# Kernel tuning notes

Hardware: AMD Instinct MI355X
Metric: run time of the kernel (lower is better)

## Reference

```python
import jax, jax.numpy as jnp
import numpy as np

# ---- dims ----
D_MODEL = 256
HEADDIM = 16          # per-head d_model for each inner Mamba2
NH = D_MODEL // HEADDIM   # 16 DiffMamba heads
D_STATE = 64
D_CONV = 4
EXPAND = 2
D_INNER = EXPAND * HEADDIM        # 32
NH_IN = D_INNER // HEADDIM        # 2 internal mamba2 heads
CONV_DIM = D_INNER + 2 * D_STATE  # 160
D_IN_PROJ = 2 * D_INNER + 2 * D_STATE + NH_IN  # 194
B, T = 2, 2048


def silu(v):
    return v * jax.nn.sigmoid(v)


def mamba2_single(u, Win, convw, convb, dt_bias, A_log, Dp, nw, Wout):
    """Reference Mamba2 forward for one module. u: [B, T, HEADDIM]."""
    Bb, Tt, _ = u.shape
    zxbcdt = u @ Win.T                       # [B, T, D_IN_PROJ]
    z = zxbcdt[..., :D_INNER]
    xBC = zxbcdt[..., D_INNER:D_INNER + CONV_DIM]
    dt = jax.nn.softplus(zxbcdt[..., -NH_IN:] + dt_bias)  # [B, T, NH_IN]
    # causal depthwise conv1d over time (kernel D_CONV)
    xp = jnp.pad(xBC, ((0, 0), (D_CONV - 1, 0), (0, 0)))
    conv = convb + sum(xp[:, k:k + Tt, :] * convw[:, k] for k in range(D_CONV))
    xBC = silu(conv)
    x = xBC[..., :D_INNER].reshape(Bb, Tt, NH_IN, HEADDIM)
    Bm = xBC[..., D_INNER:D_INNER + D_STATE]   # [B, T, N]
    Cm = xBC[..., D_INNER + D_STATE:]          # [B, T, N]
    A = -jnp.exp(A_log)                        # [NH_IN]
    dA = jnp.exp(dt * A)                       # [B, T, NH_IN]
    dBx = jnp.einsum('bth,btn,bthp->bthpn', dt, Bm, x)

    def step(h, inp):
        dA_t, dBx_t, C_t = inp                 # [B,H], [B,H,P,N], [B,N]
        h = dA_t[:, :, None, None] * h + dBx_t
        y = jnp.einsum('bhpn,bn->bhp', h, C_t)
        return h, y

    h0 = jnp.zeros((Bb, NH_IN, HEADDIM, D_STATE), u.dtype)
    xs = (jnp.moveaxis(dA, 1, 0), jnp.moveaxis(dBx, 1, 0), jnp.moveaxis(Cm, 1, 0))
    _, ys = jax.lax.scan(step, h0, xs)         # ys: [T, B, H, P]
    y = jnp.moveaxis(ys, 0, 1) + Dp[None, None, :, None] * x
    y = y.reshape(Bb, Tt, D_INNER)
    # RMSNormGated(norm_before_gate=False): gate then rmsnorm
    y = y * silu(z)
    y = y * jax.lax.rsqrt(jnp.mean(y * y, axis=-1, keepdims=True) + 1e-5) * nw
    return y @ Wout.T                          # [B, T, HEADDIM]


mamba2_v = jax.vmap(mamba2_single)  # over stacked head/module axis


def setup_inputs() -> dict:
    key = jax.random.key(0)

    def team_params(kbase, tag):
        k = jax.random.split(kbase, 6)
        Win = jax.random.uniform(k[0], (NH, D_IN_PROJ, HEADDIM), minval=-0.25, maxval=0.25)
        convw = jax.random.uniform(k[1], (NH, CONV_DIM, D_CONV), minval=-0.5, maxval=0.5)
        convb = jax.random.uniform(k[2], (NH, CONV_DIM), minval=-0.5, maxval=0.5)
        dt = jnp.exp(jax.random.uniform(k[3], (NH, NH_IN)) * (np.log(0.1) - np.log(1e-3)) + np.log(1e-3))
        dtb = jnp.log(jnp.expm1(dt))
        Alog = jnp.log(jax.random.uniform(k[4], (NH, NH_IN), minval=1.0, maxval=16.0))
        Dp = jnp.ones((NH, NH_IN))
        nw = jnp.ones((NH, D_INNER))
        Wout = jax.random.uniform(k[5], (NH, HEADDIM, D_INNER), minval=-1.0 / np.sqrt(D_INNER), maxval=1.0 / np.sqrt(D_INNER))
        return {tag + '_in': Win, tag + '_conv': convw, tag + '_convb': convb,
                tag + '_dtb': dtb, tag + '_Alog': Alog, tag + '_D': Dp,
                tag + '_nw': nw, tag + '_out': Wout}

    k = jax.random.split(key, 8)
    inp = {'x': jax.random.normal(k[0], (B, T, D_MODEL), dtype=jnp.float32)}
    inp.update(team_params(k[1], 'W1'))
    inp.update(team_params(k[2], 'W2'))
    inp['lam'] = jnp.ones((D_MODEL,))
    inp['gn_w'] = jnp.ones((NH, HEADDIM))
    inp['gn_b'] = jnp.zeros((NH, HEADDIM))
    bound = 1.0 / np.sqrt(D_MODEL)
    inp['proj_w'] = jax.random.uniform(k[3], (D_MODEL, D_MODEL), minval=-bound, maxval=bound)
    inp['proj_b'] = jax.random.uniform(k[4], (D_MODEL,), minval=-bound, maxval=bound)
    return inp


def reference(x, W1_in, W1_conv, W1_convb, W1_dtb, W1_Alog, W1_D, W1_nw, W1_out,
              W2_in, W2_conv, W2_convb, W2_dtb, W2_Alog, W2_D, W2_nw, W2_out,
              lam, gn_w, gn_b, proj_w, proj_b):
    Bb, Tt, Dm = x.shape
    # chunk into NH heads of size HEADDIM -> [NH, B, T, HEADDIM]
    xh = jnp.moveaxis(x.reshape(Bb, Tt, NH, HEADDIM), 2, 0)
    y1 = mamba2_v(xh, W1_in, W1_conv, W1_convb, W1_dtb, W1_Alog, W1_D, W1_nw, W1_out)
    y2 = mamba2_v(xh, W2_in, W2_conv, W2_convb, W2_dtb, W2_Alog, W2_D, W2_nw, W2_out)
    diff = y1 - lam.reshape(NH, 1, 1, HEADDIM) * y2   # [NH, B, T, HEADDIM]
    # GroupNorm(num_groups=1, num_channels=HEADDIM) over (C, T) per sample
    mean = jnp.mean(diff, axis=(2, 3), keepdims=True)
    var = jnp.var(diff, axis=(2, 3), keepdims=True)
    diff = (diff - mean) * jax.lax.rsqrt(var + 1e-5)
    diff = diff * gn_w[:, None, None, :] + gn_b[:, None, None, :]
    out = jnp.moveaxis(diff, 0, 2).reshape(Bb, Tt, Dm)
    return x + out @ proj_w.T + proj_b
```

## Files before the change

### kernel.cpp

```cpp
#include <hip/hip_runtime.h>
#include <math.h>

#define NHEADS 16
#define BBATCH 2
#define TSEQ   2048
#define HD     16
#define DIN    32
#define DST    64
#define CONVD  160
#define DPROJ  194
#define NHIN   2
#define DMODEL 256
#define CHUNK  32
#define NCHUNK (TSEQ / CHUNK)
#define NWG    (2 * NHEADS * BBATCH * NCHUNK)
#define NWG3   (NHEADS * BBATCH * NCHUNK)
#define YS     36

struct TeamParams {
  const float *Win, *convw, *convb, *dtb, *Alog, *Dp, *nw, *Wout;
};

typedef __attribute__((ext_vector_type(4)))  _Float16 half4;
typedef __attribute__((ext_vector_type(8)))  _Float16 half8;
typedef __attribute__((ext_vector_type(16))) float    f32x16;

__device__ __forceinline__ float sigm(float v) { return 1.0f / (1.0f + __expf(-v)); }

__device__ __forceinline__ half8 pack_h8(float4 a, float4 b) {
  half8 r;
  r[0] = (_Float16)a.x; r[1] = (_Float16)a.y; r[2] = (_Float16)a.z; r[3] = (_Float16)a.w;
  r[4] = (_Float16)b.x; r[5] = (_Float16)b.y; r[6] = (_Float16)b.z; r[7] = (_Float16)b.w;
  return r;
}
__device__ __forceinline__ half8 zero_h8() {
  half8 r;
#pragma unroll
  for (int i = 0; i < 8; ++i) r[i] = (_Float16)0.f;
  return r;
}
__device__ __forceinline__ half8 ld8(const _Float16* p) {
  const half4 a = *reinterpret_cast<const half4*>(p);
  const half4 b = *reinterpret_cast<const half4*>(p + 4);
  half8 r;
  r[0] = a[0]; r[1] = a[1]; r[2] = a[2]; r[3] = a[3];
  r[4] = b[0]; r[5] = b[1]; r[6] = b[2]; r[7] = b[3];
  return r;
}

__global__ __launch_bounds__(256, 5)
void k1_proj_ssd(const float* __restrict__ x, TeamParams tp0, TeamParams tp1,
                 _Float16* __restrict__ Sg, float* __restrict__ Pbuf,
                 float2* __restrict__ cumsg, _Float16* __restrict__ xgC,
                 _Float16* __restrict__ yintra)
{
  __shared__ _Float16 rawT[160][36];
  __shared__ _Float16 actH[32][164];
  __shared__ _Float16 Gm[2][32][36];
  __shared__ _Float16 StL[32][68];
  __shared__ float    dtraw[35][2];
  __shared__ float    clL[2][32];
  __shared__ float    dtL[2][32];

  _Float16 (*XtL)[36] = &rawT[0];
  _Float16 (*WXt)[36] = &rawT[32];
  _Float16 (*BmT)[36] = &rawT[64];

  const int tid  = threadIdx.x;
  const int wg   = blockIdx.x;
  const int c    = wg % NCHUNK;
  const int b    = (wg / NCHUNK) % BBATCH;
  const int h    = (wg / (NCHUNK * BBATCH)) % NHEADS;
  const int team = wg / (NCHUNK * BBATCH * NHEADS);
  const TeamParams P = team ? tp1 : tp0;
  const int c0 = c * CHUNK;
  const size_t base0 = ((size_t)team * NHEADS + h) * BBATCH + b;

  const int lane = tid & 63;
  const int wv   = tid >> 6;
  const int lrow = lane & 31;
  const int kg   = lane >> 5;

  half8 afr0, afr1;
  {
    const int t = c0 - 3 + lrow;
    if (t >= 0) {
      const float* xp = &x[((size_t)b * TSEQ + t) * DMODEL + h * HD + kg * 8];
      afr0 = pack_h8(*reinterpret_cast<const float4*>(xp),
                     *reinterpret_cast<const float4*>(xp + 4));
    } else afr0 = zero_h8();
    if (lrow < 3) {
      const int t1 = c0 + 29 + lrow;
      const float* xp = &x[((size_t)b * TSEQ + t1) * DMODEL + h * HD + kg * 8];
      afr1 = pack_h8(*reinterpret_cast<const float4*>(xp),
                     *reinterpret_cast<const float4*>(xp + 4));
    } else afr1 = zero_h8();
  }
  const int  tA   = (wv < 2) ? wv * 2 : (wv == 2 ? 4 : 5);
  const bool hasB = (wv < 2);
  const int  tB   = wv * 2 + 1;
  half8 bfrA, bfrB = zero_h8();
  {
    const int rA = 32 + tA * 32 + lrow;
    if (rA < DPROJ) {
      const float* wp = &P.Win[((size_t)h * DPROJ + rA) * HD + kg * 8];
      bfrA = pack_h8(*reinterpret_cast<const float4*>(wp),
                     *reinterpret_cast<const float4*>(wp + 4));
    } else bfrA = zero_h8();
    if (hasB) {
      const int rB = 32 + tB * 32 + lrow;
      const float* wp = &P.Win[((size_t)h * DPROJ + rB) * HD + kg * 8];
      bfrB = pack_h8(*reinterpret_cast<const float4*>(wp),
                     *reinterpret_cast<const float4*>(wp + 4));
    }
  }

  f32x16 z16;
#pragma unroll
  for (int i = 0; i < 16; ++i) z16[i] = 0.0f;

  auto writeD = [&](const f32x16& d, int tile, int m0) {
    if (tile < 5) {
      const int ch = tile * 32 + lrow;
      if (m0 == 0) {
#pragma unroll
        for (int m = 0; m < 4; ++m) {
          half4 v;
#pragma unroll
          for (int i = 0; i < 4; ++i) v[i] = (_Float16)d[4 * m + i];
          *reinterpret_cast<half4*>(&rawT[ch][4 * kg + 8 * m]) = v;
        }
      } else if (kg == 0) {
#pragma unroll
        for (int rg = 0; rg < 3; ++rg) rawT[ch][32 + rg] = (_Float16)d[rg];
      }
    } else if (lrow < 2) {
      if (m0 == 0) {
#pragma unroll
        for (int rg = 0; rg < 16; ++rg)
          dtraw[(rg & 3) + 8 * (rg >> 2) + 4 * kg][lrow] = d[rg];
      } else if (kg == 0) {
#pragma unroll
        for (int rg = 0; rg < 3; ++rg) dtraw[32 + rg][lrow] = d[rg];
      }
    }
  };

  {
    f32x16 d;
    d = __builtin_amdgcn_mfma_f32_32x32x16_f16(afr0, bfrA, z16, 0, 0, 0);
    writeD(d, tA, 0);
    d = __builtin_amdgcn_mfma_f32_32x32x16_f16(afr1, bfrA, z16, 0, 0, 0);
    writeD(d, tA, 1);
    if (hasB) {
      d = __builtin_amdgcn_mfma_f32_32x32x16_f16(afr0, bfrB, z16, 0, 0, 0);
      writeD(d, tB, 0);
      d = __builtin_amdgcn_mfma_f32_32x32x16_f16(afr1, bfrB, z16, 0, 0, 0);
      writeD(d, tB, 1);
    }
  }
  __syncthreads();

  const int cg = tid & 31, tg = tid >> 5;
  const int ch0 = cg * 5, t0c = tg * 4;
  float outv[5][4];
#pragma unroll
  for (int q = 0; q < 5; ++q) {
    const int ch = ch0 + q;
    const float4 cw = *reinterpret_cast<const float4*>(&P.convw[((size_t)h * CONVD + ch) * 4]);
    const float cb = P.convb[h * CONVD + ch];
    const half4 r0 = *reinterpret_cast<const half4*>(&rawT[ch][t0c]);
    const half4 r1 = *reinterpret_cast<const half4*>(&rawT[ch][t0c + 4]);
    float vv[7];
#pragma unroll
    for (int i = 0; i < 4; ++i) vv[i] = (float)r0[i];
#pragma unroll
    for (int i = 0; i < 3; ++i) vv[4 + i] = (float)r1[i];
#pragma unroll
    for (int d0 = 0; d0 < 4; ++d0) {
      float v = cb;
      v = fmaf(cw.x, vv[d0], v);
      v = fmaf(cw.y, vv[d0 + 1], v);
      v = fmaf(cw.z, vv[d0 + 2], v);
      v = fmaf(cw.w, vv[d0 + 3], v);
      outv[q][d0] = v * sigm(v);
    }
  }
  if (tid < 64) {
    const int t = tid & 31, hi = tid >> 5;
    const float dtbias = P.dtb[h * NHIN + hi];
    const float Ah = -__expf(P.Alog[h * NHIN + hi]);
    const float raw = dtraw[3 + t][hi] + dtbias;
    const float dtv = (raw > 20.f) ? raw : log1pf(__expf(raw));
    dtL[hi][t] = dtv;
    float s = dtv * Ah;
#pragma unroll
    for (int d = 1; d < 32; d <<= 1) {
      const float v = __shfl_up(s, d, 32);
      if (t >= d) s += v;
    }
    clL[hi][t] = s;
  }
  __syncthreads();

#pragma unroll
  for (int q = 0; q < 5; ++q) {
    const int ch = ch0 + q;
#pragma unroll
    for (int d0 = 0; d0 < 4; ++d0) actH[t0c + d0][ch] = (_Float16)outv[q][d0];
    if (ch < DIN) {
      const int hi = ch >> 4;
      const float cl31 = clL[hi][31];
      half4 xt, wx;
#pragma unroll
      for (int d0 = 0; d0 < 4; ++d0) {
        const int t = t0c + d0;
        const float dtv = dtL[hi][t];
        const float w = __expf(cl31 - clL[hi][t]);
        xt[d0] = (_Float16)(dtv * outv[q][d0]);
        wx[d0] = (_Float16)(w * dtv * outv[q][d0]);
      }
      *reinterpret_cast<half4*>(&XtL[ch][t0c]) = xt;
      *reinterpret_cast<half4*>(&WXt[ch][t0c]) = wx;
    } else if (ch < DIN + DST) {
      half4 bm;
#pragma unroll
      for (int d0 = 0; d0 < 4; ++d0) bm[d0] = (_Float16)outv[q][d0];
      *reinterpret_cast<half4*>(&BmT[ch - DIN][t0c]) = bm;
    }
  }
  __syncthreads();

  if (wv == 0) {
    f32x16 g;
#pragma unroll
    for (int i = 0; i < 16; ++i) g[i] = 0.0f;
#pragma unroll
    for (int kk = 0; kk < 4; ++kk) {
      const half8 af = ld8(&actH[lrow][96 + kk * 16 + kg * 8]);
      const half8 bf = ld8(&actH[lrow][32 + kk * 16 + kg * 8]);
      g = __builtin_amdgcn_mfma_f32_32x32x16_f16(af, bf, g, 0, 0, 0);
    }
    const float cls0 = clL[0][lrow], cls1 = clL[1][lrow];
#pragma unroll
    for (int rg = 0; rg < 16; ++rg) {
      const int t = (rg & 3) + 8 * (rg >> 2) + 4 * kg;
      const float gg = g[rg];
      float l0 = 0.f, l1 = 0.f;
      if (lrow <= t) { l0 = __expf(clL[0][t] - cls0); l1 = __expf(clL[1][t] - cls1); }
      Gm[0][t][lrow] = (_Float16)(l0 * gg);
      Gm[1][t][lrow] = (_Float16)(l1 * gg);
    }
  } else if (wv == 1 || wv == 2) {
    const int nhalf = (wv - 1) * 32;
    const half8 wa0 = ld8(&WXt[lrow][kg * 8]);
    const half8 wa1 = ld8(&WXt[lrow][16 + kg * 8]);
    f32x16 acc;
#pragma unroll
    for (int i = 0; i < 16; ++i) acc[i] = 0.0f;
    acc = __builtin_amdgcn_mfma_f32_32x32x16_f16(
        wa0, ld8(&BmT[nhalf + lrow][kg * 8]), acc, 0, 0, 0);
    acc = __builtin_amdgcn_mfma_f32_32x32x16_f16(
        wa1, ld8(&BmT[nhalf + lrow][16 + kg * 8]), acc, 0, 0, 0);
#pragma unroll
    for (int rg = 0; rg < 16; ++rg) {
      const int m = (rg & 3) + 8 * (rg >> 2) + 4 * kg;
      StL[m][nhalf + lrow] = (_Float16)acc[rg];
    }
  } else {
    if (lane < 32) {
      cumsg[(size_t)wg * CHUNK + lane] =
          make_float2(__expf(clL[0][lane]), __expf(clL[1][lane]));
    } else if (lane == 32) {
      Pbuf[(base0 * NCHUNK + c) * NHIN + 0] = __expf(clL[0][31]);
    } else if (lane == 33) {
      Pbuf[(base0 * NCHUNK + c) * NHIN + 1] = __expf(clL[1][31]);
    }
#pragma unroll
    for (int k = 0; k < 8; ++k) {
      const int idx = lane + k * 64;
      const int t = idx >> 4, c4 = (idx & 15) * 4;
      *reinterpret_cast<ushort4*>(&xgC[(size_t)wg * (CHUNK * DST) + t * DST + c4]) =
          *reinterpret_cast<const ushort4*>(&actH[t][96 + c4]);
    }
  }
  __syncthreads();

  if (wv < 2) {
    const int hi = wv;
    const half8 xb0 = ld8(&XtL[lrow][kg * 8]);
    const half8 xb1 = ld8(&XtL[lrow][16 + kg * 8]);
    f32x16 acc;
#pragma unroll
    for (int i = 0; i < 16; ++i) acc[i] = 0.0f;
    acc = __builtin_amdgcn_mfma_f32_32x32x16_f16(ld8(&Gm[hi][lrow][kg * 8]), xb0, acc, 0, 0, 0);
    acc = __builtin_amdgcn_mfma_f32_32x32x16_f16(ld8(&Gm[hi][lrow][16 + kg * 8]), xb1, acc, 0, 0, 0);
    const bool own = (lrow >> 4) == hi;
    if (own) {
      const float Dp = P.Dp[h * NHIN + hi];
      _Float16* yo = &yintra[(size_t)wg * (CHUNK * DIN)];
#pragma unroll
      for (int rg = 0; rg < 16; ++rg) {
        const int t = (rg & 3) + 8 * (rg >> 2) + 4 * kg;
        yo[t * DIN + lrow] = (_Float16)(acc[rg] + Dp * (float)actH[t][lrow]);
      }
    }
  } else if (wv == 2) {
    const size_t base2 = (base0 * NCHUNK + c) * (NHIN * HD * DST);
#pragma unroll
    for (int k = 0; k < 8; ++k) {
      const int idx = lane + k * 64;
      const int row = idx >> 4, c4 = (idx & 15) * 4;
      *reinterpret_cast<ushort4*>(&Sg[base2 + row * DST + c4]) =
          *reinterpret_cast<const ushort4*>(&StL[row][c4]);
    }
  }
}

__global__ __launch_bounds__(256)
void carry_kernel(_Float16* __restrict__ Sg, const float* __restrict__ Pbuf)
{
  const int wg = blockIdx.x;
  const int b = wg % BBATCH;
  const int h = (wg / BBATCH) % NHEADS;
  const int team = wg / (BBATCH * NHEADS);
  const int tid = threadIdx.x;
  const int hi = tid >> 7;
  const int pp = (tid >> 3) & 15;
  const int ng = tid & 7;
  const int nb = ng * 8;
  const size_t base0 = ((size_t)team * NHEADS + h) * BBATCH + b;

  float hc[8] = {0, 0, 0, 0, 0, 0, 0, 0};
  for (int cb = 0; cb < NCHUNK; cb += 8) {
    half8 a[8];
    float Pv[8];
#pragma unroll
    for (int j = 0; j < 8; ++j) {
      const size_t sb = (((base0 * NCHUNK + cb + j) * NHIN + hi) * HD + pp) * DST + nb;
      a[j] = *reinterpret_cast<const half8*>(&Sg[sb]);
      Pv[j] = Pbuf[(base0 * NCHUNK + cb + j) * NHIN + hi];
    }
#pragma unroll
    for (int j = 0; j < 8; ++j) {
      const size_t sb = (((base0 * NCHUNK + cb + j) * NHIN + hi) * HD + pp) * DST + nb;
      half8 o;
#pragma unroll
      for (int k = 0; k < 8; ++k) o[k] = (_Float16)hc[k];
      *reinterpret_cast<half8*>(&Sg[sb]) = o;
#pragma unroll
      for (int k = 0; k < 8; ++k) hc[k] = fmaf(Pv[j], hc[k], (float)a[j][k]);
    }
  }
}

__global__ __launch_bounds__(256)
void k3_fused(const _Float16* __restrict__ Sg, const float2* __restrict__ cumsg,
              const _Float16* __restrict__ xgC, const float* __restrict__ x,
              TeamParams tp0, TeamParams tp1,
              const _Float16* __restrict__ yintra, const float* __restrict__ lam,
              float* __restrict__ diffb, float2* __restrict__ pstat)
{
  __shared__ float    ysh[2][CHUNK][YS];
  __shared__ float    wn[2][16][33];
  __shared__ float    cums2[2][CHUNK][2];
  __shared__ _Float16 zsh[2][32][40];
  __shared__ float    youtL[2][CHUNK][20];
  __shared__ float    red2[8];

  const int tid  = threadIdx.x;
  const int wg   = blockIdx.x;
  const int c    = wg % NCHUNK;
  const int b    = (wg / NCHUNK) % BBATCH;
  const int h    = wg / (NCHUNK * BBATCH);
  const int c0 = c * CHUNK;
  const int lane = tid & 63;
  const int wv   = tid >> 6;

  const size_t wgT0 = (((size_t)0 * NHEADS + h) * BBATCH + b) * NCHUNK + c;
  const size_t wgT1 = (((size_t)1 * NHEADS + h) * BBATCH + b) * NCHUNK + c;

  f32x16 acc;
  if (wv < 2) {
    const size_t wgT = wv ? wgT1 : wgT0;
    const int colid = lane & 31, kg = lane >> 5;
    const _Float16* ca = &xgC[wgT * (CHUNK * DST) + (size_t)colid * DST + kg * 8];
    const _Float16* hb = &Sg[wgT * (NHIN * HD * DST) + (size_t)colid * DST + kg * 8];
#pragma unroll
    for (int i = 0; i < 16; ++i) acc[i] = 0.0f;
    acc = __builtin_amdgcn_mfma_f32_32x32x16_f16(
        *reinterpret_cast<const half8*>(ca), *reinterpret_cast<const half8*>(hb), acc, 0, 0, 0);
    acc = __builtin_amdgcn_mfma_f32_32x32x16_f16(
        *reinterpret_cast<const half8*>(ca + 16), *reinterpret_cast<const half8*>(hb + 16), acc, 0, 0, 0);
    acc = __builtin_amdgcn_mfma_f32_32x32x16_f16(
        *reinterpret_cast<const half8*>(ca + 32), *reinterpret_cast<const half8*>(hb + 32), acc, 0, 0, 0);
    acc = __builtin_amdgcn_mfma_f32_32x32x16_f16(
        *reinterpret_cast<const half8*>(ca + 48), *reinterpret_cast<const half8*>(hb + 48), acc, 0, 0, 0);
  } else {
    const int team = wv - 2;
    const TeamParams P = team ? tp1 : tp0;
    const int lrow = lane & 31, kg = lane >> 5;
    const float* xp = &x[((size_t)b * TSEQ + c0 + lrow) * DMODEL + h * HD + kg * 8];
    const half8 afr = pack_h8(*reinterpret_cast<const float4*>(xp),
                              *reinterpret_cast<const float4*>(xp + 4));
    const float* wp = &P.Win[((size_t)h * DPROJ + lrow) * HD + kg * 8];
    const half8 bfr = pack_h8(*reinterpret_cast<const float4*>(wp),
                              *reinterpret_cast<const float4*>(wp + 4));
    f32x16 zacc;
#pragma unroll
    for (int i = 0; i < 16; ++i) zacc[i] = 0.0f;
    zacc = __builtin_amdgcn_mfma_f32_32x32x16_f16(afr, bfr, zacc, 0, 0, 0);
#pragma unroll
    for (int rg = 0; rg < 16; ++rg) {
      const int t = (rg & 3) + 8 * (rg >> 2) + 4 * kg;
      const float v = zacc[rg];
      zsh[team][t][lrow] = (_Float16)(v * sigm(v));
    }
  }

  {
    const TeamParams P0 = tp0, P1 = tp1;
#pragma unroll
    for (int k = 0; k < 4; ++k) {
      const int i = tid + k * 256;
      const int tm = i >> 9, o = (i >> 5) & 15, dn = i & 31;
      const TeamParams& PP = tm ? P1 : P0;
      wn[tm][o][dn] = PP.Wout[((size_t)h * HD + o) * DIN + dn] * PP.nw[h * DIN + dn];
    }
  }
  {
    const int tm = tid >> 7, li = tid & 127;
    const int t = li >> 2, c8 = (li & 3) * 8;
    const size_t wgT = tm ? wgT1 : wgT0;
    const half8 v = *reinterpret_cast<const half8*>(&yintra[wgT * (CHUNK * DIN) + li * 8]);
#pragma unroll
    for (int j = 0; j < 8; ++j) ysh[tm][t][c8 + j] = (float)v[j];
  }
  if (tid < 64) {
    const int tm = tid >> 5, t = tid & 31;
    const size_t wgT = tm ? wgT1 : wgT0;
    const float2 v = cumsg[wgT * CHUNK + t];
    cums2[tm][t][0] = v.x; cums2[tm][t][1] = v.y;
  }
  __syncthreads();

  if (wv < 2) {
    const int team = wv;
    const int colid = lane & 31, kg = lane >> 5;
    const int hi = colid >> 4;
#pragma unroll
    for (int rg = 0; rg < 16; ++rg) {
      const int t = (rg & 3) + 8 * (rg >> 2) + 4 * kg;
      ysh[team][t][colid] = fmaf(cums2[team][t][hi], acc[rg], ysh[team][t][colid]);
    }
  }
  __syncthreads();

  {
    const int tm = tid >> 7, l = tid & 127;
    const int q = l & 3, tl = l >> 2;
    const int dn0 = q * 8;
    float yg[8];
    float ss = 0.0f;
#pragma unroll
    for (int j = 0; j < 8; ++j) {
      const float g = ysh[tm][tl][dn0 + j] * (float)zsh[tm][tl][dn0 + j];
      yg[j] = g;
      ss += g * g;
    }
    ss += __shfl_xor(ss, 1, 4);
    ss += __shfl_xor(ss, 2, 4);
    const float rms = rsqrtf(ss * (1.0f / DIN) + 1e-5f);
#pragma unroll
    for (int j = 0; j < 8; ++j) ysh[tm][tl][dn0 + j] = yg[j] * rms;
  }
  __syncthreads();

  {
    const int tm = tid >> 7, l = tid & 127;
    const int q = l & 3, tl = l >> 2;
#pragma unroll
    for (int oo = 0; oo < 4; ++oo) {
      const int o = q * 4 + oo;
      float a = 0.0f;
#pragma unroll
      for (int dn = 0; dn < DIN; ++dn) a = fmaf(ysh[tm][tl][dn], wn[tm][o][dn], a);
      youtL[tm][tl][o] = a;
    }
  }
  __syncthreads();

  float s = 0.0f, s2 = 0.0f;
  if (tid < 128) {
    const int t = tid >> 2, hd0 = (tid & 3) * 4;
    const float4 l4 = *reinterpret_cast<const float4*>(&lam[h * HD + hd0]);
    const float* y0 = &youtL[0][t][hd0];
    const float* y1 = &youtL[1][t][hd0];
    float4 d;
    d.x = y0[0] - l4.x * y1[0];
    d.y = y0[1] - l4.y * y1[1];
    d.z = y0[2] - l4.z * y1[2];
    d.w = y0[3] - l4.w * y1[3];
    *reinterpret_cast<float4*>(
        &diffb[(((size_t)(h * BBATCH + b)) * TSEQ + c0 + t) * HD + hd0]) = d;
    s = d.x + d.y + d.z + d.w;
    s2 = d.x * d.x + d.y * d.y + d.z * d.z + d.w * d.w;
  }
#pragma unroll
  for (int off = 1; off < 64; off <<= 1) {
    s += __shfl_xor(s, off);
    s2 += __shfl_xor(s2, off);
  }
  if (lane == 0) { red2[wv * 2] = s; red2[wv * 2 + 1] = s2; }
  __syncthreads();
  if (tid == 0) pstat[wg] = make_float2(red2[0] + red2[2], red2[1] + red2[3]);
}

#define NFW (BBATCH * (TSEQ / 32) * 2)
__global__ __launch_bounds__(256)
void final_mfma(const float* __restrict__ x, const float* __restrict__ diffb,
                const float2* __restrict__ pstat, const float* __restrict__ gnw,
                const float* __restrict__ gnb, const float* __restrict__ projw,
                const float* __restrict__ projb, float* __restrict__ out)
{
  __shared__ _Float16 ndH[32][268];
  __shared__ float statL[NHEADS][2];

  const int wg = blockIdx.x;
  const int chalf = wg & 1;
  const int tt = (wg >> 1) & 63;
  const int b = wg >> 7;
  const int t0 = tt * 32;
  const int tid = threadIdx.x;
  const int lane = tid & 63;
  const int wv = tid >> 6;

  {
    const int h = tid >> 4, k0 = tid & 15;
    float s = 0.0f, s2 = 0.0f;
    for (int k = k0; k < NCHUNK; k += 16) {
      const float2 v = pstat[((size_t)h * BBATCH + b) * NCHUNK + k];
      s += v.x; s2 += v.y;
    }
    s += __shfl_xor(s, 1, 16);  s2 += __shfl_xor(s2, 1, 16);
    s += __shfl_xor(s, 2, 16);  s2 += __shfl_xor(s2, 2, 16);
    s += __shfl_xor(s, 4, 16);  s2 += __shfl_xor(s2, 4, 16);
    s += __shfl_xor(s, 8, 16);  s2 += __shfl_xor(s2, 8, 16);
    if (k0 == 0) {
      const float inv = 1.0f / (TSEQ * HD);
      const float mean = s * inv;
      const float var = s2 * inv - mean * mean;
      statL[h][0] = mean;
      statL[h][1] = rsqrtf(var + 1e-5f);
    }
  }
  __syncthreads();

  {
    const int d = tid, h = d >> 4, hd = d & 15;
    const float mean = statL[h][0];
    const float rstd = statL[h][1];
    const float g = gnw[d];
    const float be = gnb[d];
    const float* dp = &diffb[((size_t)(h * BBATCH + b) * TSEQ + t0) * HD + hd];
#pragma unroll
    for (int t = 0; t < 32; ++t)
      ndH[t][d] = (_Float16)((dp[t * HD] - mean) * rstd * g + be);
  }
  __syncthreads();

  const int lrow = lane & 31, kg = lane >> 5;
  const int n0 = chalf * 128 + wv * 32;
  const int d = n0 + lrow;
  f32x16 acc;
#pragma unroll
  for (int i = 0; i < 16; ++i) acc[i] = 0.0f;
  const float* wp0 = &projw[(size_t)d * DMODEL + kg * 8];
#pragma unroll
  for (int kt = 0; kt < DMODEL; kt += 16) {
    const half8 af = ld8(&ndH[lrow][kt + kg * 8]);
    const half8 bf = pack_h8(*reinterpret_cast<const float4*>(wp0 + kt),
                             *reinterpret_cast<const float4*>(wp0 + kt + 4));
    acc = __builtin_amdgcn_mfma_f32_32x32x16_f16(af, bf, acc, 0, 0, 0);
  }

  const float pb = projb[d];
#pragma unroll
  for (int rg = 0; rg < 16; ++rg) {
    const int t = (rg & 3) + 8 * (rg >> 2) + 4 * kg;
    const size_t o = ((size_t)b * TSEQ + t0 + t) * DMODEL + d;
    out[o] = x[o] + pb + acc[rg];
  }
}

extern "C" void kernel_launch(void* const* d_in, const int* in_sizes, int n_in,
                              void* d_out, int out_size, void* d_ws, size_t ws_size,
                              hipStream_t stream)
{
  const float* x = (const float*)d_in[0];
  TeamParams tp0 { (const float*)d_in[1], (const float*)d_in[2], (const float*)d_in[3],
                   (const float*)d_in[4], (const float*)d_in[5], (const float*)d_in[6],
                   (const float*)d_in[7], (const float*)d_in[8] };
  TeamParams tp1 { (const float*)d_in[9], (const float*)d_in[10], (const float*)d_in[11],
                   (const float*)d_in[12], (const float*)d_in[13], (const float*)d_in[14],
                   (const float*)d_in[15], (const float*)d_in[16] };
  const float* lam   = (const float*)d_in[17];
  const float* gnw   = (const float*)d_in[18];
  const float* gnb   = (const float*)d_in[19];
  const float* projw = (const float*)d_in[20];
  const float* projb = (const float*)d_in[21];

  char* wsb = (char*)d_ws;
  _Float16* Sg    = (_Float16*)wsb;
  float* Pbuf     = (float*)(wsb + 16777216);
  float2* cumsg   = (float2*)(wsb + 16809984);
  _Float16* xgC   = (_Float16*)(wsb + 17858560);
  _Float16* yintra= (_Float16*)(wsb + 34635776);
  float* diffb    = (float*)(wsb + 43024384);
  float2* pstat   = (float2*)(wsb + 47218688);

  k1_proj_ssd<<<dim3(NWG), dim3(256), 0, stream>>>(x, tp0, tp1, Sg, Pbuf, cumsg, xgC, yintra);
  carry_kernel<<<dim3(2 * NHEADS * BBATCH), dim3(256), 0, stream>>>(Sg, Pbuf);
  k3_fused<<<dim3(NWG3), dim3(256), 0, stream>>>(Sg, cumsg, xgC, x, tp0, tp1, yintra, lam, diffb, pstat);
  final_mfma<<<dim3(NFW), dim3(256), 0, stream>>>(
      x, diffb, pstat, gnw, gnb, projw, projb, (float*)d_out);
}
```

Measured before the change: 91.08 us.

## Fold causal conv into MFMA projection and split carry scan into more blocks

The depthwise causal conv is folded into the input projection: each of the four conv taps scales the Win fragment and is accumulated by an MFMA over time-shifted x fragments. This removes the separate raw-projection shared buffer and the scalar conv pass. Work across waves is rebalanced, the dt cumsum is done per wave with shuffles, and the carry kernel now runs as 4x more 64-thread blocks, each handling a contiguous slice of the state, to get more parallelism. The cost is more MFMAs per tile, extra half-precision rounding of conv-weight times Win products, and lower occupancy bounds on k1.

```diff
diff --git a/kernel.cpp b/kernel.cpp
--- a/kernel.cpp
+++ b/kernel.cpp
@@ -48,23 +48,22 @@
   return r;
 }
 
-__global__ __launch_bounds__(256, 5)
+__global__ __launch_bounds__(256, 4)
 void k1_proj_ssd(const float* __restrict__ x, TeamParams tp0, TeamParams tp1,
                  _Float16* __restrict__ Sg, float* __restrict__ Pbuf,
                  float2* __restrict__ cumsg, _Float16* __restrict__ xgC,
                  _Float16* __restrict__ yintra)
 {
-  __shared__ _Float16 rawT[160][36];
-  __shared__ _Float16 actH[32][164];
+  __shared__ _Float16 xvT[32][36];
+  __shared__ _Float16 BmT[64][36];
+  __shared__ _Float16 actB[32][68];
+  __shared__ _Float16 actC[32][68];
+  __shared__ _Float16 XtL[32][36];
+  __shared__ _Float16 WXt[32][36];
   __shared__ _Float16 Gm[2][32][36];
   __shared__ _Float16 StL[32][68];
-  __shared__ float    dtraw[35][2];
-  __shared__ float    clL[2][32];
-  __shared__ float    dtL[2][32];
-
-  _Float16 (*XtL)[36] = &rawT[0];
-  _Float16 (*WXt)[36] = &rawT[32];
-  _Float16 (*BmT)[36] = &rawT[64];
+  __shared__ float    dtraw[32][2];
+  __shared__ float    clL[2][32], dtL2[2][32], dwL[2][32];
 
   const int tid  = threadIdx.x;
   const int wg   = blockIdx.x;
@@ -81,166 +80,139 @@
   const int lrow = lane & 31;
   const int kg   = lane >> 5;
 
-  half8 afr0, afr1;
-  {
-    const int t = c0 - 3 + lrow;
-    if (t >= 0) {
-      const float* xp = &x[((size_t)b * TSEQ + t) * DMODEL + h * HD + kg * 8];
-      afr0 = pack_h8(*reinterpret_cast<const float4*>(xp),
-                     *reinterpret_cast<const float4*>(xp + 4));
-    } else afr0 = zero_h8();
-    if (lrow < 3) {
-      const int t1 = c0 + 29 + lrow;
-      const float* xp = &x[((size_t)b * TSEQ + t1) * DMODEL + h * HD + kg * 8];
-      afr1 = pack_h8(*reinterpret_cast<const float4*>(xp),
-                     *reinterpret_cast<const float4*>(xp + 4));
-    } else afr1 = zero_h8();
-  }
-  const int  tA   = (wv < 2) ? wv * 2 : (wv == 2 ? 4 : 5);
-  const bool hasB = (wv < 2);
-  const int  tB   = wv * 2 + 1;
-  half8 bfrA, bfrB = zero_h8();
-  {
-    const int rA = 32 + tA * 32 + lrow;
-    if (rA < DPROJ) {
-      const float* wp = &P.Win[((size_t)h * DPROJ + rA) * HD + kg * 8];
-      bfrA = pack_h8(*reinterpret_cast<const float4*>(wp),
-                     *reinterpret_cast<const float4*>(wp + 4));
-    } else bfrA = zero_h8();
-    if (hasB) {
-      const int rB = 32 + tB * 32 + lrow;
-      const float* wp = &P.Win[((size_t)h * DPROJ + rB) * HD + kg * 8];
-      bfrB = pack_h8(*reinterpret_cast<const float4*>(wp),
-                     *reinterpret_cast<const float4*>(wp + 4));
-    }
-  }
-
   f32x16 z16;
 #pragma unroll
   for (int i = 0; i < 16; ++i) z16[i] = 0.0f;
-
-  auto writeD = [&](const f32x16& d, int tile, int m0) {
-    if (tile < 5) {
-      const int ch = tile * 32 + lrow;
-      if (m0 == 0) {
-#pragma unroll
-        for (int m = 0; m < 4; ++m) {
-          half4 v;
-#pragma unroll
-          for (int i = 0; i < 4; ++i) v[i] = (_Float16)d[4 * m + i];
-          *reinterpret_cast<half4*>(&rawT[ch][4 * kg + 8 * m]) = v;
-        }
-      } else if (kg == 0) {
-#pragma unroll
-        for (int rg = 0; rg < 3; ++rg) rawT[ch][32 + rg] = (_Float16)d[rg];
+  f32x16 g = z16;
+
+  half8 afr[4];
+#pragma unroll
+  for (int j = 0; j < 4; ++j) {
+    const int tp = c0 + lrow - 3 + j;
+    if (tp >= 0) {
+      const float* xp = &x[((size_t)b * TSEQ + tp) * DMODEL + h * HD + kg * 8];
+      afr[j] = pack_h8(*reinterpret_cast<const float4*>(xp),
+                       *reinterpret_cast<const float4*>(xp + 4));
+    } else afr[j] = zero_h8();
+  }
+
+  auto doTile = [&](int tile) {
+    const int ch = tile * 32 + lrow;
+    const float* wp = &P.Win[((size_t)h * DPROJ + 32 + ch) * HD + kg * 8];
+    const float4 w0 = *reinterpret_cast<const float4*>(wp);
+    const float4 w1 = *reinterpret_cast<const float4*>(wp + 4);
+    const float wf[8] = {w0.x, w0.y, w0.z, w0.w, w1.x, w1.y, w1.z, w1.w};
+    const float4 cw = *reinterpret_cast<const float4*>(&P.convw[((size_t)h * CONVD + ch) * 4]);
+    const float cwk[4] = {cw.x, cw.y, cw.z, cw.w};
+    const float cb = P.convb[h * CONVD + ch];
+    f32x16 acc = z16;
+#pragma unroll
+    for (int j = 0; j < 4; ++j) {
+      half8 bf;
+#pragma unroll
+      for (int i = 0; i < 8; ++i) bf[i] = (_Float16)(cwk[j] * wf[i]);
+      acc = __builtin_amdgcn_mfma_f32_32x32x16_f16(afr[j], bf, acc, 0, 0, 0);
+    }
+    _Float16 sv[16];
+#pragma unroll
+    for (int rg = 0; rg < 16; ++rg) {
+      const float vv = acc[rg] + cb;
+      sv[rg] = (_Float16)(vv * sigm(vv));
+    }
+    if (tile == 0) {
+#pragma unroll
+      for (int m = 0; m < 4; ++m) {
+        half4 v; v[0] = sv[4*m]; v[1] = sv[4*m+1]; v[2] = sv[4*m+2]; v[3] = sv[4*m+3];
+        *reinterpret_cast<half4*>(&xvT[lrow][4 * kg + 8 * m]) = v;
       }
-    } else if (lrow < 2) {
-      if (m0 == 0) {
-#pragma unroll
-        for (int rg = 0; rg < 16; ++rg)
-          dtraw[(rg & 3) + 8 * (rg >> 2) + 4 * kg][lrow] = d[rg];
-      } else if (kg == 0) {
-#pragma unroll
-        for (int rg = 0; rg < 3; ++rg) dtraw[32 + rg][lrow] = d[rg];
+    } else if (tile <= 2) {
+      const int n = ch - 32;
+#pragma unroll
+      for (int m = 0; m < 4; ++m) {
+        half4 v; v[0] = sv[4*m]; v[1] = sv[4*m+1]; v[2] = sv[4*m+2]; v[3] = sv[4*m+3];
+        *reinterpret_cast<half4*>(&BmT[n][4 * kg + 8 * m]) = v;
       }
+#pragma unroll
+      for (int rg = 0; rg < 16; ++rg) {
+        const int t = (rg & 3) + 8 * (rg >> 2) + 4 * kg;
+        actB[t][n] = sv[rg];
+      }
+    } else {
+      const int n = ch - 96;
+#pragma unroll
+      for (int rg = 0; rg < 16; ++rg) {
+        const int t = (rg & 3) + 8 * (rg >> 2) + 4 * kg;
+        actC[t][n] = sv[rg];
+      }
     }
   };
 
-  {
-    f32x16 d;
-    d = __builtin_amdgcn_mfma_f32_32x32x16_f16(afr0, bfrA, z16, 0, 0, 0);
-    writeD(d, tA, 0);
-    d = __builtin_amdgcn_mfma_f32_32x32x16_f16(afr1, bfrA, z16, 0, 0, 0);
-    writeD(d, tA, 1);
-    if (hasB) {
-      d = __builtin_amdgcn_mfma_f32_32x32x16_f16(afr0, bfrB, z16, 0, 0, 0);
-      writeD(d, tB, 0);
-      d = __builtin_amdgcn_mfma_f32_32x32x16_f16(afr1, bfrB, z16, 0, 0, 0);
-      writeD(d, tB, 1);
-    }
-  }
-  __syncthreads();
-
-  const int cg = tid & 31, tg = tid >> 5;
-  const int ch0 = cg * 5, t0c = tg * 4;
-  float outv[5][4];
-#pragma unroll
-  for (int q = 0; q < 5; ++q) {
-    const int ch = ch0 + q;
-    const float4 cw = *reinterpret_cast<const float4*>(&P.convw[((size_t)h * CONVD + ch) * 4]);
-    const float cb = P.convb[h * CONVD + ch];
-    const half4 r0 = *reinterpret_cast<const half4*>(&rawT[ch][t0c]);
-    const half4 r1 = *reinterpret_cast<const half4*>(&rawT[ch][t0c + 4]);
-    float vv[7];
-#pragma unroll
-    for (int i = 0; i < 4; ++i) vv[i] = (float)r0[i];
-#pragma unroll
-    for (int i = 0; i < 3; ++i) vv[4 + i] = (float)r1[i];
-#pragma unroll
-    for (int d0 = 0; d0 < 4; ++d0) {
-      float v = cb;
-      v = fmaf(cw.x, vv[d0], v);
-      v = fmaf(cw.y, vv[d0 + 1], v);
-      v = fmaf(cw.z, vv[d0 + 2], v);
-      v = fmaf(cw.w, vv[d0 + 3], v);
-      outv[q][d0] = v * sigm(v);
-    }
-  }
-  if (tid < 64) {
-    const int t = tid & 31, hi = tid >> 5;
+  if (wv == 0) {
+    doTile(0);
+    half8 bf5 = zero_h8();
+    if (lrow < 2) {
+      const float* wp = &P.Win[((size_t)h * DPROJ + 192 + lrow) * HD + kg * 8];
+      bf5 = pack_h8(*reinterpret_cast<const float4*>(wp),
+                    *reinterpret_cast<const float4*>(wp + 4));
+    }
+    const f32x16 a5 = __builtin_amdgcn_mfma_f32_32x32x16_f16(afr[3], bf5, z16, 0, 0, 0);
+    if (lrow < 2) {
+#pragma unroll
+      for (int rg = 0; rg < 16; ++rg) {
+        const int t = (rg & 3) + 8 * (rg >> 2) + 4 * kg;
+        dtraw[t][lrow] = a5[rg];
+      }
+    }
+  } else if (wv == 1) {
+    doTile(1);
+  } else if (wv == 2) {
+    doTile(2);
+  } else {
+    doTile(3);
+    doTile(4);
+  }
+  __syncthreads();
+
+  if (wv == 0) {
+#pragma unroll
+    for (int kk = 0; kk < 4; ++kk) {
+      const half8 af = ld8(&actC[lrow][kk * 16 + kg * 8]);
+      const half8 bf = ld8(&actB[lrow][kk * 16 + kg * 8]);
+      g = __builtin_amdgcn_mfma_f32_32x32x16_f16(af, bf, g, 0, 0, 0);
+    }
+  } else if (wv == 1) {
+    const int t = lane & 31, hi = lane >> 5;
     const float dtbias = P.dtb[h * NHIN + hi];
     const float Ah = -__expf(P.Alog[h * NHIN + hi]);
-    const float raw = dtraw[3 + t][hi] + dtbias;
+    const float raw = dtraw[t][hi] + dtbias;
     const float dtv = (raw > 20.f) ? raw : log1pf(__expf(raw));
-    dtL[hi][t] = dtv;
     float s = dtv * Ah;
 #pragma unroll
     for (int d = 1; d < 32; d <<= 1) {
       const float v = __shfl_up(s, d, 32);
       if (t >= d) s += v;
     }
+    const float cl31 = __shfl(s, 31, 32);
+    const float w = __expf(cl31 - s);
+    const float ecl = __expf(s);
     clL[hi][t] = s;
-  }
-  __syncthreads();
-
-#pragma unroll
-  for (int q = 0; q < 5; ++q) {
-    const int ch = ch0 + q;
-#pragma unroll
-    for (int d0 = 0; d0 < 4; ++d0) actH[t0c + d0][ch] = (_Float16)outv[q][d0];
-    if (ch < DIN) {
-      const int hi = ch >> 4;
-      const float cl31 = clL[hi][31];
-      half4 xt, wx;
-#pragma unroll
-      for (int d0 = 0; d0 < 4; ++d0) {
-        const int t = t0c + d0;
-        const float dtv = dtL[hi][t];
-        const float w = __expf(cl31 - clL[hi][t]);
-        xt[d0] = (_Float16)(dtv * outv[q][d0]);
-        wx[d0] = (_Float16)(w * dtv * outv[q][d0]);
-      }
-      *reinterpret_cast<half4*>(&XtL[ch][t0c]) = xt;
-      *reinterpret_cast<half4*>(&WXt[ch][t0c]) = wx;
-    } else if (ch < DIN + DST) {
-      half4 bm;
-#pragma unroll
-      for (int d0 = 0; d0 < 4; ++d0) bm[d0] = (_Float16)outv[q][d0];
-      *reinterpret_cast<half4*>(&BmT[ch - DIN][t0c]) = bm;
+    dtL2[hi][t] = dtv;
+    dwL[hi][t] = w * dtv;
+    const float eo = __shfl(ecl, (lane & 31) + 32, 64);
+    if (lane < 32) cumsg[(size_t)wg * CHUNK + t] = make_float2(ecl, eo);
+    if (t == 31) Pbuf[(base0 * NCHUNK + c) * NHIN + hi] = ecl;
+  } else if (wv == 2) {
+#pragma unroll
+    for (int k = 0; k < 8; ++k) {
+      const int idx = lane + k * 64;
+      const int t = idx >> 4, c4 = (idx & 15) * 4;
+      *reinterpret_cast<ushort4*>(&xgC[(size_t)wg * (CHUNK * DST) + t * DST + c4]) =
+          *reinterpret_cast<const ushort4*>(&actC[t][c4]);
     }
   }
   __syncthreads();
 
   if (wv == 0) {
-    f32x16 g;
-#pragma unroll
-    for (int i = 0; i < 16; ++i) g[i] = 0.0f;
-#pragma unroll
-    for (int kk = 0; kk < 4; ++kk) {
-      const half8 af = ld8(&actH[lrow][96 + kk * 16 + kg * 8]);
-      const half8 bf = ld8(&actH[lrow][32 + kk * 16 + kg * 8]);
-      g = __builtin_amdgcn_mfma_f32_32x32x16_f16(af, bf, g, 0, 0, 0);
-    }
     const float cls0 = clL[0][lrow], cls1 = clL[1][lrow];
 #pragma unroll
     for (int rg = 0; rg < 16; ++rg) {
@@ -252,12 +224,48 @@
       Gm[1][t][lrow] = (_Float16)(l1 * gg);
     }
   } else if (wv == 1 || wv == 2) {
+    const int idx = tid - 64;
+    const int ch = idx & 31, tq = idx >> 5;
+    const int hi = ch >> 4;
+#pragma unroll
+    for (int hh = 0; hh < 2; ++hh) {
+      const int t4 = tq * 8 + hh * 4;
+      const half4 xv4 = *reinterpret_cast<const half4*>(&xvT[ch][t4]);
+      half4 xt, wx;
+#pragma unroll
+      for (int i = 0; i < 4; ++i) {
+        const int t = t4 + i;
+        const float xv = (float)xv4[i];
+        xt[i] = (_Float16)(dtL2[hi][t] * xv);
+        wx[i] = (_Float16)(dwL[hi][t] * xv);
+      }
+      *reinterpret_cast<half4*>(&XtL[ch][t4]) = xt;
+      *reinterpret_cast<half4*>(&WXt[ch][t4]) = wx;
+    }
+  }
+  __syncthreads();
+
+  if (wv == 0 || wv == 3) {
+    const int hi = (wv == 0) ? 0 : 1;
+    const half8 xb0 = ld8(&XtL[lrow][kg * 8]);
+    const half8 xb1 = ld8(&XtL[lrow][16 + kg * 8]);
+    f32x16 acc = z16;
+    acc = __builtin_amdgcn_mfma_f32_32x32x16_f16(ld8(&Gm[hi][lrow][kg * 8]), xb0, acc, 0, 0, 0);
+    acc = __builtin_amdgcn_mfma_f32_32x32x16_f16(ld8(&Gm[hi][lrow][16 + kg * 8]), xb1, acc, 0, 0, 0);
+    if ((lrow >> 4) == hi) {
+      const float Dp = P.Dp[h * NHIN + hi];
+      _Float16* yo = &yintra[(size_t)wg * (CHUNK * DIN)];
+#pragma unroll
+      for (int rg = 0; rg < 16; ++rg) {
+        const int t = (rg & 3) + 8 * (rg >> 2) + 4 * kg;
+        yo[t * DIN + lrow] = (_Float16)(acc[rg] + Dp * (float)xvT[lrow][t]);
+      }
+    }
+  } else {
     const int nhalf = (wv - 1) * 32;
     const half8 wa0 = ld8(&WXt[lrow][kg * 8]);
     const half8 wa1 = ld8(&WXt[lrow][16 + kg * 8]);
-    f32x16 acc;
-#pragma unroll
-    for (int i = 0; i < 16; ++i) acc[i] = 0.0f;
+    f32x16 acc = z16;
     acc = __builtin_amdgcn_mfma_f32_32x32x16_f16(
         wa0, ld8(&BmT[nhalf + lrow][kg * 8]), acc, 0, 0, 0);
     acc = __builtin_amdgcn_mfma_f32_32x32x16_f16(
@@ -267,68 +275,34 @@
       const int m = (rg & 3) + 8 * (rg >> 2) + 4 * kg;
       StL[m][nhalf + lrow] = (_Float16)acc[rg];
     }
-  } else {
-    if (lane < 32) {
-      cumsg[(size_t)wg * CHUNK + lane] =
-          make_float2(__expf(clL[0][lane]), __expf(clL[1][lane]));
-    } else if (lane == 32) {
-      Pbuf[(base0 * NCHUNK + c) * NHIN + 0] = __expf(clL[0][31]);
-    } else if (lane == 33) {
-      Pbuf[(base0 * NCHUNK + c) * NHIN + 1] = __expf(clL[1][31]);
-    }
-#pragma unroll
-    for (int k = 0; k < 8; ++k) {
+  }
+  __syncthreads();
+
+  if (wv == 1 || wv == 2) {
+    const int nhalf = (wv - 1) * 32;
+    const size_t base2 = (base0 * NCHUNK + c) * (NHIN * HD * DST);
+#pragma unroll
+    for (int k = 0; k < 4; ++k) {
       const int idx = lane + k * 64;
-      const int t = idx >> 4, c4 = (idx & 15) * 4;
-      *reinterpret_cast<ushort4*>(&xgC[(size_t)wg * (CHUNK * DST) + t * DST + c4]) =
-          *reinterpret_cast<const ushort4*>(&actH[t][96 + c4]);
-    }
-  }
-  __syncthreads();
-
-  if (wv < 2) {
-    const int hi = wv;
-    const half8 xb0 = ld8(&XtL[lrow][kg * 8]);
-    const half8 xb1 = ld8(&XtL[lrow][16 + kg * 8]);
-    f32x16 acc;
-#pragma unroll
-    for (int i = 0; i < 16; ++i) acc[i] = 0.0f;
-    acc = __builtin_amdgcn_mfma_f32_32x32x16_f16(ld8(&Gm[hi][lrow][kg * 8]), xb0, acc, 0, 0, 0);
-    acc = __builtin_amdgcn_mfma_f32_32x32x16_f16(ld8(&Gm[hi][lrow][16 + kg * 8]), xb1, acc, 0, 0, 0);
-    const bool own = (lrow >> 4) == hi;
-    if (own) {
-      const float Dp = P.Dp[h * NHIN + hi];
-      _Float16* yo = &yintra[(size_t)wg * (CHUNK * DIN)];
-#pragma unroll
-      for (int rg = 0; rg < 16; ++rg) {
-        const int t = (rg & 3) + 8 * (rg >> 2) + 4 * kg;
-        yo[t * DIN + lrow] = (_Float16)(acc[rg] + Dp * (float)actH[t][lrow]);
-      }
-    }
-  } else if (wv == 2) {
-    const size_t base2 = (base0 * NCHUNK + c) * (NHIN * HD * DST);
-#pragma unroll
-    for (int k = 0; k < 8; ++k) {
-      const int idx = lane + k * 64;
-      const int row = idx >> 4, c4 = (idx & 15) * 4;
+      const int row = idx >> 3, c4 = (idx & 7) * 4 + nhalf;
       *reinterpret_cast<ushort4*>(&Sg[base2 + row * DST + c4]) =
           *reinterpret_cast<const ushort4*>(&StL[row][c4]);
     }
   }
 }
 
-__global__ __launch_bounds__(256)
+__global__ __launch_bounds__(64)
 void carry_kernel(_Float16* __restrict__ Sg, const float* __restrict__ Pbuf)
 {
   const int wg = blockIdx.x;
-  const int b = wg % BBATCH;
-  const int h = (wg / BBATCH) % NHEADS;
-  const int team = wg / (BBATCH * NHEADS);
-  const int tid = threadIdx.x;
-  const int hi = tid >> 7;
-  const int pp = (tid >> 3) & 15;
-  const int ng = tid & 7;
-  const int nb = ng * 8;
+  const int q = wg & 3;
+  const int rest = wg >> 2;
+  const int b = rest % BBATCH;
+  const int h = (rest / BBATCH) % NHEADS;
+  const int team = rest / (BBATCH * NHEADS);
+  const int lane = threadIdx.x;
+  const int off = q * 512 + lane * 8;
+  const int hi = q >> 1;
   const size_t base0 = ((size_t)team * NHEADS + h) * BBATCH + b;
 
   float hc[8] = {0, 0, 0, 0, 0, 0, 0, 0};
@@ -337,13 +311,13 @@
     float Pv[8];
 #pragma unroll
     for (int j = 0; j < 8; ++j) {
-      const size_t sb = (((base0 * NCHUNK + cb + j) * NHIN + hi) * HD + pp) * DST + nb;
+      const size_t sb = (base0 * NCHUNK + cb + j) * (NHIN * HD * DST) + off;
       a[j] = *reinterpret_cast<const half8*>(&Sg[sb]);
       Pv[j] = Pbuf[(base0 * NCHUNK + cb + j) * NHIN + hi];
     }
 #pragma unroll
     for (int j = 0; j < 8; ++j) {
-      const size_t sb = (((base0 * NCHUNK + cb + j) * NHIN + hi) * HD + pp) * DST + nb;
+      const size_t sb = (base0 * NCHUNK + cb + j) * (NHIN * HD * DST) + off;
       half8 o;
 #pragma unroll
       for (int k = 0; k < 8; ++k) o[k] = (_Float16)hc[k];
@@ -620,7 +594,7 @@
   float2* pstat   = (float2*)(wsb + 47218688);
 
   k1_proj_ssd<<<dim3(NWG), dim3(256), 0, stream>>>(x, tp0, tp1, Sg, Pbuf, cumsg, xgC, yintra);
-  carry_kernel<<<dim3(2 * NHEADS * BBATCH), dim3(256), 0, stream>>>(Sg, Pbuf);
+  carry_kernel<<<dim3(2 * NHEADS * BBATCH * 4), dim3(64), 0, stream>>>(Sg, Pbuf);
   k3_fused<<<dim3(NWG3), dim3(256), 0, stream>>>(Sg, cumsg, xgC, x, tp0, tp1, yintra, lam, diffb, pstat);
   final_mfma<<<dim3(NFW), dim3(256), 0, stream>>>(
       x, diffb, pstat, gnw, gnb, projw, projb, (float*)d_out);
```

New measurement: 88.98 us. -2.3%, faster.
